# Kernel tuning notes

Hardware: AMD Instinct MI355X
Metric: run time of the kernel (lower is better)

Reference implementation:

```python
import jax, jax.numpy as jnp
import numpy as np

V, D, L, H, SLOTS, FF = 32000, 1024, 6, 16, 4096, 4096
DH = D // H

def rmsnorm(x, w, eps=1e-8):
    return x * jax.lax.rsqrt(jnp.mean(x * x, axis=-1, keepdims=True) + eps) * w

def rope(x):
    # x: [B,T,D]; interleaved RoPE over full d_model as in RoPEEmbedding
    T = x.shape[1]
    inv_freq = 1.0 / (10000.0 ** (jnp.arange(0, D, 2, dtype=jnp.float32) / D))
    freqs = jnp.arange(T, dtype=jnp.float32)[:, None] * inv_freq[None, :]  # [T, D/2]
    cos, sin = jnp.cos(freqs), jnp.sin(freqs)
    x1, x2 = x[..., ::2], x[..., 1::2]
    out = jnp.stack([x1 * cos - x2 * sin, x1 * sin + x2 * cos], axis=-1)
    return out.reshape(x.shape)

def block(x, Wq, Wk, Wv, Wo, bo, n1, Wg, Wu, Wd, n2):
    B, T, _ = x.shape
    q = (x @ Wq).reshape(B, T, H, DH)
    k = (x @ Wk).reshape(B, T, H, DH)
    v = (x @ Wv).reshape(B, T, H, DH)
    scores = jnp.einsum('bqhd,bkhd->bhqk', q, k) * (DH ** -0.5)
    attn = jax.nn.softmax(scores, axis=-1)
    o = jnp.einsum('bhqk,bkhd->bqhd', attn, v).reshape(B, T, D)
    x = rmsnorm(x + o @ Wo + bo, n1)
    ff = (jax.nn.silu(x @ Wg) * (x @ Wu)) @ Wd
    return rmsnorm(x + ff, n2)

def setup_inputs() -> dict:
    key = jax.random.key(0)
    ks = jax.random.split(key, 20)
    nrm = lambda k, s: (jax.random.normal(k, s, jnp.float32) * 0.02)
    inp = {
        'ids': jax.random.randint(ks[0], (2, 2048), 0, V),
        'tok_embed': nrm(ks[1], (V, D)),
        'Wq': nrm(ks[2], (L, D, D)), 'Wk': nrm(ks[3], (L, D, D)),
        'Wv': nrm(ks[4], (L, D, D)), 'Wo': nrm(ks[5], (L, D, D)),
        'bo': jnp.zeros((L, D), jnp.float32),
        'n1': jnp.ones((L, D), jnp.float32),
        'Wg': nrm(ks[6], (L, D, FF)), 'Wu': nrm(ks[7], (L, D, FF)),
        'Wd': nrm(ks[8], (L, FF, D)),
        'n2': jnp.ones((L, D), jnp.float32),
        'mem': nrm(ks[9], (SLOTS, D)),
        'Wsp': nrm(ks[10], (D, D)), 'bsp': jnp.zeros((D,), jnp.float32),
        'Wrp': nrm(ks[11], (D, D)), 'brp': jnp.zeros((D,), jnp.float32),
        'nout': jnp.ones((D,), jnp.float32),
    }
    return inp

def reference(ids, tok_embed, Wq, Wk, Wv, Wo, bo, n1, Wg, Wu, Wd, n2,
              mem, Wsp, bsp, Wrp, brp, nout):
    x = tok_embed[ids]            # [B,T,D] gather
    x = rope(x)
    for i in range(L):
        x = block(x, Wq[i], Wk[i], Wv[i], Wo[i], bo[i], n1[i],
                  Wg[i], Wu[i], Wd[i], n2[i])
    # StateBank content-addressed read: route queries over memory slots
    q = x @ Wsp + bsp                                   # [B,T,D]
    slot_scores = jnp.einsum('btd,sd->bts', q, mem) * (D ** -0.5)
    attention_maps = jax.nn.softmax(slot_scores, axis=-1)  # [B,T,SLOTS]
    r = jnp.einsum('bts,sd->btd', attention_maps, mem)     # gather-route read
    r = r @ Wrp + brp
    h = rmsnorm(x + r, nout)
    logits = h @ tok_embed.T      # tied lm_head
    return logits
```

## Files before the change

kernel.cpp:

```cpp
#include <hip/hip_runtime.h>

typedef __bf16 bf16;
typedef __attribute__((ext_vector_type(8))) __bf16 bf16x8;
typedef __attribute__((ext_vector_type(4))) __bf16 bf16x4;
typedef __attribute__((ext_vector_type(4))) float f32x4;

#define NL 6
#define DIM 1024
#define NH 16
#define DH 64
#define TT 2048
#define BB 2
#define BT 4096
#define FFD 4096
#define NSLOT 4096
#define NV 32000

__device__ __forceinline__ void gld16(const void* g, void* l) {
  __builtin_amdgcn_global_load_lds(
      (const __attribute__((address_space(1))) void*)g,
      (__attribute__((address_space(3))) void*)l, 16, 0, 0);
}


__global__ void cvt_bf16(const float* __restrict__ s, bf16* __restrict__ d, long n) {
  long i = ((long)blockIdx.x * 256 + threadIdx.x) * 4;
  if (i + 3 < n) {
    float4 v = *(const float4*)(s + i);
    bf16x4 o = {(bf16)v.x, (bf16)v.y, (bf16)v.z, (bf16)v.w};
    *(bf16x4*)(d + i) = o;
  }
}

__global__ void transpose_cvt(const float* __restrict__ src, bf16* __restrict__ dst, int R, int C) {
  __shared__ float tile[32][33];
  int c0 = blockIdx.x * 32, r0 = blockIdx.y * 32;
  int tx = threadIdx.x;
  int ty = threadIdx.y;
  float4 v = *(const float4*)(src + (size_t)(r0 + ty) * C + c0 + tx * 4);
  tile[ty][tx * 4 + 0] = v.x;
  tile[ty][tx * 4 + 1] = v.y;
  tile[ty][tx * 4 + 2] = v.z;
  tile[ty][tx * 4 + 3] = v.w;
  __syncthreads();
  bf16x4 o = {(bf16)tile[tx * 4 + 0][ty], (bf16)tile[tx * 4 + 1][ty],
              (bf16)tile[tx * 4 + 2][ty], (bf16)tile[tx * 4 + 3][ty]};
  *(bf16x4*)(dst + (size_t)(c0 + ty) * R + r0 + tx * 4) = o;
}

__global__ void transpose_v(const bf16* __restrict__ v, int ldv, bf16* __restrict__ vT) {
  __shared__ bf16 tile[32][33];
  int t0 = blockIdx.x * 32, d0 = blockIdx.y * 32, bh = blockIdx.z;
  int b = bh >> 4, h = bh & 15;
  int tx = threadIdx.x, ty = threadIdx.y;
#pragma unroll
  for (int i = 0; i < 4; ++i)
    tile[ty + i * 8][tx] = v[(size_t)(b * TT + t0 + ty + i * 8) * ldv + h * DH + d0 + tx];
  __syncthreads();
#pragma unroll
  for (int i = 0; i < 4; ++i)
    vT[((size_t)bh * DH + d0 + ty + i * 8) * TT + t0 + tx] = tile[tx][ty + i * 8];
}


__global__ void embed_rope(const int* __restrict__ ids, const float* __restrict__ emb,
                           float* __restrict__ xf, bf16* __restrict__ xb) {
  int bt = blockIdx.x;
  int t = bt & (TT - 1);
  int id = ids[bt];
  const float* row = emb + (size_t)id * DIM;
  for (int p = threadIdx.x; p < DIM / 2; p += 256) {
    float x1 = row[2 * p], x2 = row[2 * p + 1];
    float inv = __expf(-9.210340371976184f * (float)p * (1.0f / 512.0f));
    float ang = (float)t * inv;
    float c = cosf(ang), s = sinf(ang);
    float o1 = x1 * c - x2 * s;
    float o2 = x1 * s + x2 * c;
    size_t base = (size_t)bt * DIM + 2 * p;
    xf[base] = o1; xf[base + 1] = o2;
    xb[base] = (bf16)o1; xb[base + 1] = (bf16)o2;
  }
}

enum { EP_BF16 = 0, EP_F32 = 1, EP_F32_BIAS = 2, EP_BF16_BIAS = 3, EP_SILU_MUL = 4 };


template <int EP>
__global__ __launch_bounds__(512, 1) void gemm8(
    const bf16* __restrict__ A, const bf16* __restrict__ Bt, void* __restrict__ Cp,
    const float* __restrict__ bias, const bf16* __restrict__ aux,
    int M, int N, int K) {
  __shared__ bf16 S[4][2][256 * 32];

  const int tid = threadIdx.x;
  const int lane = tid & 63;
  const int r16 = lane & 15, hi = lane >> 4;
  const int wave = tid >> 6;
  const int wm = wave >> 2, wn = wave & 3;

  const int nwg = gridDim.x;
  const int orig = blockIdx.x;
  const int qq = nwg >> 3, rr = nwg & 7;
  const int xcd = orig & 7, cidx = orig >> 3;
  const int wg = (xcd < rr ? xcd * (qq + 1) : rr * (qq + 1) + (xcd - rr) * qq) + cidx;
  const int gM = M / 256;
  const int m0 = (wg % gM) * 256;
  const int n0 = (wg / gM) * 256;

  const int srow = tid >> 2;
  const int ccol = tid & 3;
  const int skey = (srow >> 1) & 3;
  const int gcol = (ccol ^ skey) * 8;
  const bf16* aS = A + (size_t)(m0 + srow) * K + gcol;
  const bf16* bS = Bt + (size_t)(n0 + srow) * K + gcol;
  const int dst0 = tid * 8;

  const int rkey = (r16 >> 1) & 3;
  const int rchunk = (hi ^ rkey) * 8;

  f32x4 acc[8][4] = {};
  const int NT = K / 32;

#pragma unroll
  for (int s = 0; s < 3; ++s) {
    gld16(aS + s * 32, &S[s][0][dst0]);
    gld16(aS + s * 32 + (size_t)128 * K, &S[s][0][dst0 + 4096]);
    gld16(bS + s * 32, &S[s][1][dst0]);
    gld16(bS + s * 32 + (size_t)128 * K, &S[s][1][dst0 + 4096]);
  }
  asm volatile("s_waitcnt vmcnt(8)" ::: "memory");
  __builtin_amdgcn_s_barrier();
  __builtin_amdgcn_sched_barrier(0);

  for (int s = 0; s < NT; ++s) {
    const int cs = s & 3, ps = (s + 3) & 3;
    const bool pre = (s + 3) < NT;
    const bf16* SA = S[cs][0];
    const bf16* SB = S[cs][1];
    const size_t koff = (size_t)(s + 3) * 32;
    bf16x8 af[4], bfr[4];

#pragma unroll
    for (int j = 0; j < 4; ++j)
      bfr[j] = *(const bf16x8*)&SB[(wn * 64 + j * 16 + r16) * 32 + rchunk];
#pragma unroll
    for (int i = 0; i < 4; ++i)
      af[i] = *(const bf16x8*)&SA[(wm * 128 + i * 16 + r16) * 32 + rchunk];
    if (pre) {
      gld16(aS + koff, &S[ps][0][dst0]);
      gld16(aS + koff + (size_t)128 * K, &S[ps][0][dst0 + 4096]);
    }
    __builtin_amdgcn_s_barrier();
    __builtin_amdgcn_sched_barrier(0);
    __builtin_amdgcn_s_setprio(1);
#pragma unroll
    for (int i = 0; i < 4; ++i)
#pragma unroll
      for (int j = 0; j < 4; ++j)
        acc[i][j] = __builtin_amdgcn_mfma_f32_16x16x32_bf16(af[i], bfr[j], acc[i][j], 0, 0, 0);
    __builtin_amdgcn_s_setprio(0);
    __builtin_amdgcn_s_barrier();
    __builtin_amdgcn_sched_barrier(0);

#pragma unroll
    for (int i = 0; i < 4; ++i)
      af[i] = *(const bf16x8*)&SA[(wm * 128 + 64 + i * 16 + r16) * 32 + rchunk];
    if (pre) {
      gld16(bS + koff, &S[ps][1][dst0]);
      gld16(bS + koff + (size_t)128 * K, &S[ps][1][dst0 + 4096]);
    }
    __builtin_amdgcn_s_barrier();
    __builtin_amdgcn_sched_barrier(0);
    __builtin_amdgcn_s_setprio(1);
#pragma unroll
    for (int i = 0; i < 4; ++i)
#pragma unroll
      for (int j = 0; j < 4; ++j)
        acc[4 + i][j] = __builtin_amdgcn_mfma_f32_16x16x32_bf16(af[i], bfr[j], acc[4 + i][j], 0, 0, 0);
    __builtin_amdgcn_s_setprio(0);
    if (pre)               asm volatile("s_waitcnt vmcnt(8)" ::: "memory");
    else if ((s + 2) < NT) asm volatile("s_waitcnt vmcnt(4)" ::: "memory");
    else if ((s + 1) < NT) asm volatile("s_waitcnt vmcnt(0)" ::: "memory");
    __builtin_amdgcn_s_barrier();
    __builtin_amdgcn_sched_barrier(0);
  }

#pragma unroll
  for (int mi = 0; mi < 8; ++mi) {
    const int m = m0 + wm * 128 + mi * 16 + hi * 4;
#pragma unroll
    for (int j = 0; j < 4; ++j) {
      const int n = n0 + wn * 64 + j * 16 + r16;
#pragma unroll
      for (int q = 0; q < 4; ++q) {
        size_t idx = (size_t)(m + q) * N + n;
        float v = acc[mi][j][q];
        if constexpr (EP == EP_F32) {
          ((float*)Cp)[idx] = v;
        } else if constexpr (EP == EP_F32_BIAS) {
          ((float*)Cp)[idx] = v + bias[n];
        } else if constexpr (EP == EP_BF16) {
          ((bf16*)Cp)[idx] = (bf16)v;
        } else if constexpr (EP == EP_BF16_BIAS) {
          ((bf16*)Cp)[idx] = (bf16)(v + bias[n]);
        } else {
          float sg = v / (1.0f + __expf(-v));
          ((bf16*)Cp)[idx] = (bf16)(sg * (float)aux[idx]);
        }
      }
    }
  }
}


template <int BM, int BN, int WMW, int WNW, int EP>
__global__ __launch_bounds__(WMW * WNW * 64, 2) void gemmk(
    const bf16* __restrict__ A, const bf16* __restrict__ Bt, void* __restrict__ Cp,
    const float* __restrict__ bias, const bf16* __restrict__ aux,
    int M, int N, int K) {
  constexpr int BK = 32;
  constexpr int MF = BM / (WMW * 16);
  constexpr int NF = BN / (WNW * 16);
  constexpr int LA = BM / 64;
  constexpr int LB = BN / 64;
  constexpr int VM_MAIN = 2 * LA + LB;
  constexpr int VM_TAIL = LA + LB;
  __shared__ bf16 sA[4][BM * BK];
  __shared__ bf16 sB[4][BN * BK];

  const int tid = threadIdx.x;
  const int lane = tid & 63;
  const int r16 = lane & 15, hi = lane >> 4;
  const int wave = tid >> 6;
  const int wm = wave / WNW, wn = wave % WNW;

  const int nwg = gridDim.x;
  const int orig = blockIdx.x;
  const int qq = nwg >> 3, rr = nwg & 7;
  const int xcd = orig & 7, cidx = orig >> 3;
  const int wg = (xcd < rr ? xcd * (qq + 1) : rr * (qq + 1) + (xcd - rr) * qq) + cidx;
  const int gM = M / BM;
  const int m0 = (wg % gM) * BM;
  const int n0 = (wg / gM) * BN;

  const int srow = tid >> 2;
  const int ccol = tid & 3;
  const int skey = (srow >> 1) & 3;
  const int gcol = ((ccol ^ skey)) * 8;
  const bf16* aS = A + (size_t)(m0 + srow) * K + gcol;
  const bf16* bS = Bt + (size_t)(n0 + srow) * K + gcol;
  const int dst0 = srow * BK + ccol * 8;

  const int rkey = (r16 >> 1) & 3;
  const int rchunk = (hi ^ rkey) * 8;

  f32x4 acc[MF][NF] = {};
  const int NT = K / BK;

#pragma unroll
  for (int t0_ = 0; t0_ < 2; ++t0_) {
#pragma unroll
    for (int p = 0; p < LA; ++p)
      gld16(aS + t0_ * BK + (size_t)p * 64 * K, &sA[t0_][dst0 + p * 64 * BK]);
#pragma unroll
    for (int p = 0; p < LB; ++p)
      gld16(bS + t0_ * BK + (size_t)p * 64 * K, &sB[t0_][dst0 + p * 64 * BK]);
  }

  for (int t = 0; t < NT; ++t) {
    const int cb = t & 3;
    const int pb = (t + 2) & 3;
    const bool pre = (t + 2) < NT;
    if (pre) {
#pragma unroll
      for (int p = 0; p < LA; ++p)
        gld16(aS + (size_t)(t + 2) * BK + (size_t)p * 64 * K, &sA[pb][dst0 + p * 64 * BK]);
    }
    if (pre)             asm volatile("s_waitcnt vmcnt(%0)" :: "i"(VM_MAIN) : "memory");
    else if (t + 1 < NT) asm volatile("s_waitcnt vmcnt(%0)" :: "i"(VM_TAIL) : "memory");
    else                 asm volatile("s_waitcnt vmcnt(0)" ::: "memory");
    __builtin_amdgcn_s_barrier();
    __builtin_amdgcn_sched_barrier(0);

    bf16x8 bf_[NF];
#pragma unroll
    for (int j = 0; j < NF; ++j)
      bf_[j] = *(const bf16x8*)&sB[cb][(wn * (NF * 16) + j * 16 + r16) * BK + rchunk];
    if (pre) {
#pragma unroll
      for (int p = 0; p < LB; ++p)
        gld16(bS + (size_t)(t + 2) * BK + (size_t)p * 64 * K, &sB[pb][dst0 + p * 64 * BK]);
    }
    bf16x8 af[MF];
#pragma unroll
    for (int i = 0; i < MF; ++i)
      af[i] = *(const bf16x8*)&sA[cb][(wm * (MF * 16) + i * 16 + r16) * BK + rchunk];
    __builtin_amdgcn_s_setprio(1);
#pragma unroll
    for (int i = 0; i < MF; ++i)
#pragma unroll
      for (int j = 0; j < NF; ++j)
        acc[i][j] = __builtin_amdgcn_mfma_f32_16x16x32_bf16(af[i], bf_[j], acc[i][j], 0, 0, 0);
    __builtin_amdgcn_s_setprio(0);
  }

#pragma unroll
  for (int i = 0; i < MF; ++i) {
    const int m = m0 + wm * (MF * 16) + i * 16 + hi * 4;
#pragma unroll
    for (int j = 0; j < NF; ++j) {
      const int n = n0 + wn * (NF * 16) + j * 16 + r16;
#pragma unroll
      for (int q = 0; q < 4; ++q) {
        size_t idx = (size_t)(m + q) * N + n;
        float v = acc[i][j][q];
        if constexpr (EP == EP_F32) {
          ((float*)Cp)[idx] = v;
        } else if constexpr (EP == EP_F32_BIAS) {
          ((float*)Cp)[idx] = v + bias[n];
        } else if constexpr (EP == EP_BF16) {
          ((bf16*)Cp)[idx] = (bf16)v;
        } else if constexpr (EP == EP_BF16_BIAS) {
          ((bf16*)Cp)[idx] = (bf16)(v + bias[n]);
        } else {
          float sg = v / (1.0f + __expf(-v));
          ((bf16*)Cp)[idx] = (bf16)(sg * (float)aux[idx]);
        }
      }
    }
  }
}


__global__ __launch_bounds__(256, 2) void attn_flash(
    const bf16* __restrict__ Qp, const bf16* __restrict__ Kp, int ldk,
    const bf16* __restrict__ Vt, bf16* __restrict__ Op) {
  __shared__ bf16 Ks[2][128 * 32];
  __shared__ bf16 Vs[4][64 * 32];
  __shared__ bf16 Ps[4][4][16 * 40];
  const int tid = threadIdx.x, lane = tid & 63, wave = tid >> 6;
  const int h = blockIdx.y, b = blockIdx.z;
  const int r16 = lane & 15, hi = lane >> 4;
  const int qrow = blockIdx.x * 64 + wave * 16 + r16;

  bf16x8 qa[2];
  {
    const bf16* qp = Qp + (size_t)(b * TT + qrow) * ldk + h * DH + hi * 8;
    qa[0] = *(const bf16x8*)qp;
    qa[1] = *(const bf16x8*)(qp + 32);
  }
  const bf16* kBase = Kp + (size_t)(b * TT) * ldk + h * DH;
  const bf16* vBase = Vt + (size_t)(b * NH + h) * DH * TT;

  const int srow = tid >> 2, ccol = tid & 3;
  const int skey = (srow >> 1) & 3;
  const int scolS = (ccol ^ skey) * 8;
  const int dstc = ccol * 8;
  const int rkey = (r16 >> 1) & 3;
  const int rchunk = (hi ^ rkey) * 8;

  float m_run[4] = {-1e30f, -1e30f, -1e30f, -1e30f};
  float l_run[4] = {0.f, 0.f, 0.f, 0.f};
  f32x4 oacc[4] = {};

  for (int kt = 0; kt < TT; kt += 128) {
#pragma unroll
    for (int half = 0; half < 2; ++half) {
      gld16(kBase + (size_t)(kt + srow) * ldk + half * 32 + scolS, &Ks[half][srow * 32 + dstc]);
      gld16(kBase + (size_t)(kt + 64 + srow) * ldk + half * 32 + scolS, &Ks[half][(64 + srow) * 32 + dstc]);
    }
#pragma unroll
    for (int ks = 0; ks < 4; ++ks)
      gld16(vBase + (size_t)srow * TT + kt + ks * 32 + scolS, &Vs[ks][srow * 32 + dstc]);
    __syncthreads();

    f32x4 s[8];
#pragma unroll
    for (int kg = 0; kg < 8; ++kg) {
      f32x4 z = {};
      bf16x8 kb0 = *(const bf16x8*)&Ks[0][(kg * 16 + r16) * 32 + rchunk];
      bf16x8 kb1 = *(const bf16x8*)&Ks[1][(kg * 16 + r16) * 32 + rchunk];
      z = __builtin_amdgcn_mfma_f32_16x16x32_bf16(qa[0], kb0, z, 0, 0, 0);
      z = __builtin_amdgcn_mfma_f32_16x16x32_bf16(qa[1], kb1, z, 0, 0, 0);
      s[kg] = z * 0.125f;
    }
#pragma unroll
    for (int i = 0; i < 4; ++i) {
      float pm = s[0][i];
#pragma unroll
      for (int kg = 1; kg < 8; ++kg) pm = fmaxf(pm, s[kg][i]);
      pm = fmaxf(pm, __shfl_xor(pm, 1));
      pm = fmaxf(pm, __shfl_xor(pm, 2));
      pm = fmaxf(pm, __shfl_xor(pm, 4));
      pm = fmaxf(pm, __shfl_xor(pm, 8));
      float mnew = fmaxf(m_run[i], pm);
      float sc = __expf(m_run[i] - mnew);
      m_run[i] = mnew;
      l_run[i] *= sc;
#pragma unroll
      for (int n = 0; n < 4; ++n) oacc[n][i] *= sc;
#pragma unroll
      for (int kg = 0; kg < 8; ++kg) {
        float p = __expf(s[kg][i] - mnew);
        l_run[i] += p;
        Ps[wave][kg >> 1][(hi * 4 + i) * 40 + (kg & 1) * 16 + r16] = (bf16)p;
      }
    }
#pragma unroll
    for (int ks = 0; ks < 4; ++ks) {
      bf16x8 pa = *(const bf16x8*)&Ps[wave][ks][r16 * 40 + hi * 8];
#pragma unroll
      for (int n = 0; n < 4; ++n) {
        bf16x8 vb = *(const bf16x8*)&Vs[ks][(n * 16 + r16) * 32 + rchunk];
        oacc[n] = __builtin_amdgcn_mfma_f32_16x16x32_bf16(pa, vb, oacc[n], 0, 0, 0);
      }
    }
    __syncthreads();
  }

#pragma unroll
  for (int i = 0; i < 4; ++i) {
    float l = l_run[i];
    l += __shfl_xor(l, 1);
    l += __shfl_xor(l, 2);
    l += __shfl_xor(l, 4);
    l += __shfl_xor(l, 8);
    float inv = 1.0f / l;
    int trow = blockIdx.x * 64 + wave * 16 + hi * 4 + i;
    size_t base = ((size_t)b * TT + trow) * DIM + h * DH;
#pragma unroll
    for (int n = 0; n < 4; ++n)
      Op[base + n * 16 + r16] = (bf16)(oacc[n][i] * inv);
  }
}


__global__ __launch_bounds__(256) void resid_rms(
    const float* __restrict__ xin, const float* __restrict__ y, const float* __restrict__ wgt,
    float* __restrict__ xf_out, bf16* __restrict__ xb_out) {
  __shared__ float red[4];
  const int r = blockIdx.x, tid = threadIdx.x;
  const size_t base = (size_t)r * DIM + tid * 4;
  float4 v = *(const float4*)(xin + base);
  float4 u = *(const float4*)(y + base);
  v.x += u.x; v.y += u.y; v.z += u.z; v.w += u.w;
  float ss = v.x * v.x + v.y * v.y + v.z * v.z + v.w * v.w;
#pragma unroll
  for (int d = 1; d < 64; d <<= 1) ss += __shfl_xor(ss, d);
  if ((tid & 63) == 0) red[tid >> 6] = ss;
  __syncthreads();
  ss = red[0] + red[1] + red[2] + red[3];
  float sc = rsqrtf(ss * (1.0f / DIM) + 1e-8f);
  const float4 wv = *(const float4*)(wgt + tid * 4);
  float o0 = v.x * sc * wv.x, o1 = v.y * sc * wv.y, o2 = v.z * sc * wv.z, o3 = v.w * sc * wv.w;
  if (xf_out) {
    float4 ov = {o0, o1, o2, o3};
    *(float4*)(xf_out + base) = ov;
  }
  bf16x4 ob = {(bf16)o0, (bf16)o1, (bf16)o2, (bf16)o3};
  *(bf16x4*)(xb_out + base) = ob;
}


__global__ __launch_bounds__(256) void softmax_rows(const float* __restrict__ Sc, bf16* __restrict__ P) {
  __shared__ float red[4];
  const int r = blockIdx.x, tid = threadIdx.x;
  const float* row = Sc + (size_t)r * NSLOT;
  float4 v[4];
#pragma unroll
  for (int i = 0; i < 4; ++i) v[i] = *(const float4*)(row + tid * 4 + i * 1024);
  float mx = -1e30f;
#pragma unroll
  for (int i = 0; i < 4; ++i)
    mx = fmaxf(fmaxf(fmaxf(fmaxf(mx, v[i].x), v[i].y), v[i].z), v[i].w);
#pragma unroll
  for (int d = 1; d < 64; d <<= 1) mx = fmaxf(mx, __shfl_xor(mx, d));
  if ((tid & 63) == 0) red[tid >> 6] = mx;
  __syncthreads();
  mx = fmaxf(fmaxf(red[0], red[1]), fmaxf(red[2], red[3]));
  __syncthreads();
  float e[16];
  float sum = 0.f;
#pragma unroll
  for (int i = 0; i < 4; ++i) {
    e[i * 4 + 0] = __expf((v[i].x - mx) * 0.03125f);
    e[i * 4 + 1] = __expf((v[i].y - mx) * 0.03125f);
    e[i * 4 + 2] = __expf((v[i].z - mx) * 0.03125f);
    e[i * 4 + 3] = __expf((v[i].w - mx) * 0.03125f);
    sum += e[i * 4 + 0] + e[i * 4 + 1] + e[i * 4 + 2] + e[i * 4 + 3];
  }
#pragma unroll
  for (int d = 1; d < 64; d <<= 1) sum += __shfl_xor(sum, d);
  if ((tid & 63) == 0) red[tid >> 6] = sum;
  __syncthreads();
  sum = red[0] + red[1] + red[2] + red[3];
  float inv = 1.0f / sum;
#pragma unroll
  for (int i = 0; i < 4; ++i) {
    bf16x4 ob = {(bf16)(e[i * 4 + 0] * inv), (bf16)(e[i * 4 + 1] * inv),
                 (bf16)(e[i * 4 + 2] * inv), (bf16)(e[i * 4 + 3] * inv)};
    *(bf16x4*)(P + (size_t)r * NSLOT + tid * 4 + i * 1024) = ob;
  }
}


extern "C" void kernel_launch(void* const* d_in, const int* in_sizes, int n_in,
                              void* d_out, int out_size, void* d_ws, size_t ws_size,
                              hipStream_t stream) {
  (void)in_sizes; (void)n_in; (void)out_size;
  const int* ids = (const int*)d_in[0];
  const float* emb = (const float*)d_in[1];
  const float* Wq = (const float*)d_in[2];
  const float* Wk = (const float*)d_in[3];
  const float* Wv = (const float*)d_in[4];
  const float* Wo = (const float*)d_in[5];
  const float* bo = (const float*)d_in[6];
  const float* n1 = (const float*)d_in[7];
  const float* Wg = (const float*)d_in[8];
  const float* Wu = (const float*)d_in[9];
  const float* Wd = (const float*)d_in[10];
  const float* n2 = (const float*)d_in[11];
  const float* memp = (const float*)d_in[12];
  const float* Wsp = (const float*)d_in[13];
  const float* bsp = (const float*)d_in[14];
  const float* Wrp = (const float*)d_in[15];
  const float* brp = (const float*)d_in[16];
  const float* nout = (const float*)d_in[17];

  char* w = (char*)d_ws;
  auto alloc = [&](size_t bytes) -> void* {
    void* p = (void*)w;
    w += (bytes + 255) & ~(size_t)255;
    return p;
  };

  const size_t dd = (size_t)DIM * DIM;
  const size_t dff = (size_t)DIM * FFD;

  bf16* tok_b = (bf16*)alloc((size_t)NV * DIM * 2);
  bf16* mem_b = (bf16*)alloc((size_t)NSLOT * DIM * 2);
  bf16* memT  = (bf16*)alloc((size_t)NSLOT * DIM * 2);
  bf16* WspT  = (bf16*)alloc(dd * 2);
  bf16* WrpT  = (bf16*)alloc(dd * 2);
  float* xf   = (float*)alloc((size_t)BT * DIM * 4);
  bf16* xb    = (bf16*)alloc((size_t)BT * DIM * 2);
  float* yb   = (float*)alloc((size_t)BT * DIM * 4);
  bf16* W3T   = (bf16*)alloc(3 * dd * 2);
  bf16* WoT   = (bf16*)alloc(dd * 2);
  bf16* WgT   = (bf16*)alloc(dff * 2);
  bf16* WuT   = (bf16*)alloc(dff * 2);
  bf16* WdT   = (bf16*)alloc(dff * 2);
  bf16* qkv   = (bf16*)alloc((size_t)BT * 3 * DIM * 2);
  bf16* vT_   = (bf16*)alloc((size_t)BT * DIM * 2);
  bf16* ot_   = (bf16*)alloc((size_t)BT * DIM * 2);
  bf16* qb    = (bf16*)alloc((size_t)BT * DIM * 2);
  bf16* rb    = (bf16*)alloc((size_t)BT * DIM * 2);
  bf16* hb    = (bf16*)alloc((size_t)BT * DIM * 2);

  size_t used = (size_t)(w - (char*)d_ws);
  size_t region_bytes = (size_t)BT * NSLOT * 4 + (size_t)BT * NSLOT * 2;
  char* region;
  if (used + region_bytes <= ws_size) region = (char*)alloc(region_bytes);
  else region = (char*)d_out;
  bf16* Ub = (bf16*)region;
  bf16* Hb = (bf16*)(region + (size_t)BT * FFD * 2);
  float* scoresF = (float*)region;
  bf16* attnb = (bf16*)(region + (size_t)BT * NSLOT * 4);

  dim3 blkT(8, 32);
  dim3 blkV(32, 8);

  cvt_bf16<<<NV * DIM / 1024, 256, 0, stream>>>(emb, tok_b, (long)NV * DIM);
  cvt_bf16<<<NSLOT * DIM / 1024, 256, 0, stream>>>(memp, mem_b, (long)NSLOT * DIM);
  transpose_cvt<<<dim3(DIM / 32, NSLOT / 32), blkT, 0, stream>>>(memp, memT, NSLOT, DIM);
  transpose_cvt<<<dim3(DIM / 32, DIM / 32), blkT, 0, stream>>>(Wsp, WspT, DIM, DIM);
  transpose_cvt<<<dim3(DIM / 32, DIM / 32), blkT, 0, stream>>>(Wrp, WrpT, DIM, DIM);
  embed_rope<<<BT, 256, 0, stream>>>(ids, emb, xf, xb);

  for (int l = 0; l < NL; ++l) {
    transpose_cvt<<<dim3(32, 32), blkT, 0, stream>>>(Wq + l * dd, W3T, DIM, DIM);
    transpose_cvt<<<dim3(32, 32), blkT, 0, stream>>>(Wk + l * dd, W3T + dd, DIM, DIM);
    transpose_cvt<<<dim3(32, 32), blkT, 0, stream>>>(Wv + l * dd, W3T + 2 * dd, DIM, DIM);
    transpose_cvt<<<dim3(32, 32), blkT, 0, stream>>>(Wo + l * dd, WoT, DIM, DIM);
    transpose_cvt<<<dim3(FFD / 32, DIM / 32), blkT, 0, stream>>>(Wg + l * dff, WgT, DIM, FFD);
    transpose_cvt<<<dim3(FFD / 32, DIM / 32), blkT, 0, stream>>>(Wu + l * dff, WuT, DIM, FFD);
    transpose_cvt<<<dim3(DIM / 32, FFD / 32), blkT, 0, stream>>>(Wd + l * dff, WdT, FFD, DIM);

    gemm8<EP_BF16><<<dim3(16 * 12), 512, 0, stream>>>(
        xb, W3T, qkv, nullptr, nullptr, BT, 3 * DIM, DIM);
    transpose_v<<<dim3(TT / 32, DH / 32, BB * NH), blkV, 0, stream>>>(qkv + 2 * DIM, 3 * DIM, vT_);
    attn_flash<<<dim3(TT / 64, NH, BB), 256, 0, stream>>>(qkv, qkv + DIM, 3 * DIM, vT_, ot_);
    gemmk<128, 64, 2, 2, EP_F32_BIAS><<<dim3(32 * 16), 256, 0, stream>>>(
        ot_, WoT, yb, bo + l * DIM, nullptr, BT, DIM, DIM);
    resid_rms<<<BT, 256, 0, stream>>>(xf, yb, n1 + l * DIM, xf, xb);
    gemm8<EP_BF16><<<dim3(16 * 16), 512, 0, stream>>>(
        xb, WuT, Ub, nullptr, nullptr, BT, FFD, DIM);
    gemm8<EP_SILU_MUL><<<dim3(16 * 16), 512, 0, stream>>>(
        xb, WgT, Hb, nullptr, Ub, BT, FFD, DIM);
    gemmk<128, 64, 2, 2, EP_F32><<<dim3(32 * 16), 256, 0, stream>>>(
        Hb, WdT, yb, nullptr, nullptr, BT, DIM, FFD);
    resid_rms<<<BT, 256, 0, stream>>>(xf, yb, n2 + l * DIM, xf, xb);
  }

  gemmk<128, 64, 2, 2, EP_BF16_BIAS><<<dim3(32 * 16), 256, 0, stream>>>(
      xb, WspT, qb, bsp, nullptr, BT, DIM, DIM);
  gemm8<EP_F32><<<dim3(16 * 16), 512, 0, stream>>>(
      qb, mem_b, scoresF, nullptr, nullptr, BT, NSLOT, DIM);
  softmax_rows<<<BT, 256, 0, stream>>>(scoresF, attnb);
  gemmk<128, 64, 2, 2, EP_BF16><<<dim3(32 * 16), 256, 0, stream>>>(
      attnb, memT, rb, nullptr, nullptr, BT, DIM, NSLOT);
  gemmk<128, 64, 2, 2, EP_F32_BIAS><<<dim3(32 * 16), 256, 0, stream>>>(
      rb, WrpT, yb, brp, nullptr, BT, DIM, DIM);
  resid_rms<<<BT, 256, 0, stream>>>(xf, yb, nout, nullptr, hb);
  gemm8<EP_F32><<<dim3(16 * 125), 512, 0, stream>>>(
      hb, tok_b, (float*)d_out, nullptr, nullptr, BT, NV, DIM);
}
```

Baseline: 2.831 ms.

## Overlap next K/V tile loads with softmax and PV compute in attention

Restructures the flash-attention loop so that the next K tile is loaded into LDS after QK^T finishes and the next V tile after PV finishes. Partial vmcnt waits and raw s_barriers replace the full __syncthreads, so global-to-LDS traffic can overlap with the softmax and MFMA work. It also raises wave priority around the MFMA sections. The risk is subtle LDS hazards from reusing single buffers, and the extra barriers may add stalls.

```diff
diff --git a/kernel.cpp b/kernel.cpp
--- a/kernel.cpp
+++ b/kernel.cpp
@@ -363,18 +363,24 @@
   float l_run[4] = {0.f, 0.f, 0.f, 0.f};
   f32x4 oacc[4] = {};
 
+#pragma unroll
+  for (int half = 0; half < 2; ++half) {
+    gld16(kBase + (size_t)srow * ldk + half * 32 + scolS, &Ks[half][srow * 32 + dstc]);
+    gld16(kBase + (size_t)(64 + srow) * ldk + half * 32 + scolS, &Ks[half][(64 + srow) * 32 + dstc]);
+  }
+#pragma unroll
+  for (int ks = 0; ks < 4; ++ks)
+    gld16(vBase + (size_t)srow * TT + ks * 32 + scolS, &Vs[ks][srow * 32 + dstc]);
+  asm volatile("s_waitcnt vmcnt(4)" ::: "memory");
+  __builtin_amdgcn_s_barrier();
+  __builtin_amdgcn_sched_barrier(0);
+
   for (int kt = 0; kt < TT; kt += 128) {
-#pragma unroll
-    for (int half = 0; half < 2; ++half) {
-      gld16(kBase + (size_t)(kt + srow) * ldk + half * 32 + scolS, &Ks[half][srow * 32 + dstc]);
-      gld16(kBase + (size_t)(kt + 64 + srow) * ldk + half * 32 + scolS, &Ks[half][(64 + srow) * 32 + dstc]);
-    }
-#pragma unroll
-    for (int ks = 0; ks < 4; ++ks)
-      gld16(vBase + (size_t)srow * TT + kt + ks * 32 + scolS, &Vs[ks][srow * 32 + dstc]);
-    __syncthreads();
+    const bool pre = (kt + 128) < TT;
+    const int ktn = kt + 128;
 
     f32x4 s[8];
+    __builtin_amdgcn_s_setprio(1);
 #pragma unroll
     for (int kg = 0; kg < 8; ++kg) {
       f32x4 z = {};
@@ -383,6 +389,17 @@
       z = __builtin_amdgcn_mfma_f32_16x16x32_bf16(qa[0], kb0, z, 0, 0, 0);
       z = __builtin_amdgcn_mfma_f32_16x16x32_bf16(qa[1], kb1, z, 0, 0, 0);
       s[kg] = z * 0.125f;
+    }
+    __builtin_amdgcn_s_setprio(0);
+    __builtin_amdgcn_s_barrier();
+    __builtin_amdgcn_sched_barrier(0);
+
+    if (pre) {
+#pragma unroll
+      for (int half = 0; half < 2; ++half) {
+        gld16(kBase + (size_t)(ktn + srow) * ldk + half * 32 + scolS, &Ks[half][srow * 32 + dstc]);
+        gld16(kBase + (size_t)(ktn + 64 + srow) * ldk + half * 32 + scolS, &Ks[half][(64 + srow) * 32 + dstc]);
+      }
     }
 #pragma unroll
     for (int i = 0; i < 4; ++i) {
@@ -406,6 +423,12 @@
         Ps[wave][kg >> 1][(hi * 4 + i) * 40 + (kg & 1) * 16 + r16] = (bf16)p;
       }
     }
+    if (pre) asm volatile("s_waitcnt vmcnt(4)" ::: "memory");
+    else     asm volatile("s_waitcnt vmcnt(0)" ::: "memory");
+    __builtin_amdgcn_s_barrier();
+    __builtin_amdgcn_sched_barrier(0);
+
+    __builtin_amdgcn_s_setprio(1);
 #pragma unroll
     for (int ks = 0; ks < 4; ++ks) {
       bf16x8 pa = *(const bf16x8*)&Ps[wave][ks][r16 * 40 + hi * 8];
@@ -415,7 +438,18 @@
         oacc[n] = __builtin_amdgcn_mfma_f32_16x16x32_bf16(pa, vb, oacc[n], 0, 0, 0);
       }
     }
-    __syncthreads();
+    __builtin_amdgcn_s_setprio(0);
+    __builtin_amdgcn_s_barrier();
+    __builtin_amdgcn_sched_barrier(0);
+
+    if (pre) {
+#pragma unroll
+      for (int ks = 0; ks < 4; ++ks)
+        gld16(vBase + (size_t)srow * TT + ktn + ks * 32 + scolS, &Vs[ks][srow * 32 + dstc]);
+      asm volatile("s_waitcnt vmcnt(4)" ::: "memory");
+      __builtin_amdgcn_s_barrier();
+      __builtin_amdgcn_sched_barrier(0);
+    }
   }
 
 #pragma unroll
```

Measured after the change: 2.851 ms. No clear change (+0.7%).

## Restructure flash attention softmax: transposed scores, exp2, lazy rescale, setprio

Applied to the files above, without the earlier changes.

Computes S transposed (K as A operand) so each lane holds one query row's scores, which reduces the per-row max to two cross-lane shuffles instead of per-element reductions. Folds the 1/sqrt(d) scale and log2(e) into Q up front so exp2f can replace expf. Skips the accumulator rescale when the running max has not grown past a threshold, and raises wave priority around the MFMA sections. The P tile layout changes to a single padded buffer per wave. Risks: Q rounds to bf16 after scaling, and the deferred rescale bounds how large the exponents can grow.

```diff
diff --git a/kernel.cpp b/kernel.cpp
--- a/kernel.cpp
+++ b/kernel.cpp
@@ -337,17 +337,23 @@
     const bf16* __restrict__ Vt, bf16* __restrict__ Op) {
   __shared__ bf16 Ks[2][128 * 32];
   __shared__ bf16 Vs[4][64 * 32];
-  __shared__ bf16 Ps[4][4][16 * 40];
+  __shared__ bf16 Ps[4][16 * 144];
   const int tid = threadIdx.x, lane = tid & 63, wave = tid >> 6;
   const int h = blockIdx.y, b = blockIdx.z;
   const int r16 = lane & 15, hi = lane >> 4;
   const int qrow = blockIdx.x * 64 + wave * 16 + r16;
 
+  const float QS = 0.1803368801f;
   bf16x8 qa[2];
   {
     const bf16* qp = Qp + (size_t)(b * TT + qrow) * ldk + h * DH + hi * 8;
-    qa[0] = *(const bf16x8*)qp;
-    qa[1] = *(const bf16x8*)(qp + 32);
+    bf16x8 q0 = *(const bf16x8*)qp;
+    bf16x8 q1 = *(const bf16x8*)(qp + 32);
+#pragma unroll
+    for (int e = 0; e < 8; ++e) {
+      qa[0][e] = (bf16)((float)q0[e] * QS);
+      qa[1][e] = (bf16)((float)q1[e] * QS);
+    }
   }
   const bf16* kBase = Kp + (size_t)(b * TT) * ldk + h * DH;
   const bf16* vBase = Vt + (size_t)(b * NH + h) * DH * TT;
@@ -359,8 +365,8 @@
   const int rkey = (r16 >> 1) & 3;
   const int rchunk = (hi ^ rkey) * 8;
 
-  float m_run[4] = {-1e30f, -1e30f, -1e30f, -1e30f};
-  float l_run[4] = {0.f, 0.f, 0.f, 0.f};
+  float m_run = -1e30f;
+  float l_run = 0.f;
   f32x4 oacc[4] = {};
 
   for (int kt = 0; kt < TT; kt += 128) {
@@ -375,62 +381,78 @@
     __syncthreads();
 
     f32x4 s[8];
+    __builtin_amdgcn_s_setprio(1);
 #pragma unroll
     for (int kg = 0; kg < 8; ++kg) {
       f32x4 z = {};
       bf16x8 kb0 = *(const bf16x8*)&Ks[0][(kg * 16 + r16) * 32 + rchunk];
       bf16x8 kb1 = *(const bf16x8*)&Ks[1][(kg * 16 + r16) * 32 + rchunk];
-      z = __builtin_amdgcn_mfma_f32_16x16x32_bf16(qa[0], kb0, z, 0, 0, 0);
-      z = __builtin_amdgcn_mfma_f32_16x16x32_bf16(qa[1], kb1, z, 0, 0, 0);
-      s[kg] = z * 0.125f;
-    }
-#pragma unroll
-    for (int i = 0; i < 4; ++i) {
-      float pm = s[0][i];
-#pragma unroll
-      for (int kg = 1; kg < 8; ++kg) pm = fmaxf(pm, s[kg][i]);
-      pm = fmaxf(pm, __shfl_xor(pm, 1));
-      pm = fmaxf(pm, __shfl_xor(pm, 2));
-      pm = fmaxf(pm, __shfl_xor(pm, 4));
-      pm = fmaxf(pm, __shfl_xor(pm, 8));
-      float mnew = fmaxf(m_run[i], pm);
-      float sc = __expf(m_run[i] - mnew);
-      m_run[i] = mnew;
-      l_run[i] *= sc;
-#pragma unroll
-      for (int n = 0; n < 4; ++n) oacc[n][i] *= sc;
-#pragma unroll
-      for (int kg = 0; kg < 8; ++kg) {
-        float p = __expf(s[kg][i] - mnew);
-        l_run[i] += p;
-        Ps[wave][kg >> 1][(hi * 4 + i) * 40 + (kg & 1) * 16 + r16] = (bf16)p;
+      z = __builtin_amdgcn_mfma_f32_16x16x32_bf16(kb0, qa[0], z, 0, 0, 0);
+      z = __builtin_amdgcn_mfma_f32_16x16x32_bf16(kb1, qa[1], z, 0, 0, 0);
+      s[kg] = z;
+    }
+    __builtin_amdgcn_s_setprio(0);
+
+    float pm = s[0][0];
+#pragma unroll
+    for (int kg = 0; kg < 8; ++kg)
+#pragma unroll
+      for (int i = 0; i < 4; ++i) pm = fmaxf(pm, s[kg][i]);
+    pm = fmaxf(pm, __shfl_xor(pm, 16));
+    pm = fmaxf(pm, __shfl_xor(pm, 32));
+
+    if (!__all(pm - m_run <= 11.5411f)) {
+      float mnew = fmaxf(m_run, pm);
+      float f = exp2f(m_run - mnew);
+      m_run = mnew;
+      l_run *= f;
+#pragma unroll
+      for (int i = 0; i < 4; ++i) {
+        float fi = __shfl(f, hi * 4 + i);
+#pragma unroll
+        for (int n = 0; n < 4; ++n) oacc[n][i] *= fi;
       }
     }
+
+    float lsum = 0.f;
+#pragma unroll
+    for (int kg = 0; kg < 8; ++kg) {
+      float p0 = exp2f(s[kg][0] - m_run);
+      float p1 = exp2f(s[kg][1] - m_run);
+      float p2 = exp2f(s[kg][2] - m_run);
+      float p3 = exp2f(s[kg][3] - m_run);
+      lsum += (p0 + p1) + (p2 + p3);
+      bf16x4 pk = {(bf16)p0, (bf16)p1, (bf16)p2, (bf16)p3};
+      *(bf16x4*)&Ps[wave][r16 * 144 + kg * 16 + hi * 4] = pk;
+    }
+    l_run += lsum;
+
+    __builtin_amdgcn_s_setprio(1);
 #pragma unroll
     for (int ks = 0; ks < 4; ++ks) {
-      bf16x8 pa = *(const bf16x8*)&Ps[wave][ks][r16 * 40 + hi * 8];
+      bf16x8 pa = *(const bf16x8*)&Ps[wave][r16 * 144 + ks * 32 + hi * 8];
 #pragma unroll
       for (int n = 0; n < 4; ++n) {
         bf16x8 vb = *(const bf16x8*)&Vs[ks][(n * 16 + r16) * 32 + rchunk];
         oacc[n] = __builtin_amdgcn_mfma_f32_16x16x32_bf16(pa, vb, oacc[n], 0, 0, 0);
       }
     }
+    __builtin_amdgcn_s_setprio(0);
     __syncthreads();
   }
 
+  float lq = l_run;
+  lq += __shfl_xor(lq, 16);
+  lq += __shfl_xor(lq, 32);
+  float invq = 1.0f / lq;
 #pragma unroll
   for (int i = 0; i < 4; ++i) {
-    float l = l_run[i];
-    l += __shfl_xor(l, 1);
-    l += __shfl_xor(l, 2);
-    l += __shfl_xor(l, 4);
-    l += __shfl_xor(l, 8);
-    float inv = 1.0f / l;
+    float inv_i = __shfl(invq, hi * 4 + i);
     int trow = blockIdx.x * 64 + wave * 16 + hi * 4 + i;
     size_t base = ((size_t)b * TT + trow) * DIM + h * DH;
 #pragma unroll
     for (int n = 0; n < 4; ++n)
-      Op[base + n * 16 + r16] = (bf16)(oacc[n][i] * inv);
+      Op[base + n * 16 + r16] = (bf16)(oacc[n][i] * inv_i);
   }
 }
 
```

Measured after the change: 2.778 ms. Within noise of the previous version (-1.9%).
